# Kernel optimization log

Measured on AMD Instinct MI355X. Metric: run time of the kernel, lower is better.

## Reference

```python
import jax, jax.numpy as jnp
import numpy as np

BETA = 0.25  # commitment_beta


def setup_inputs() -> dict:
    key = jax.random.key(0)
    k1, k2 = jax.random.split(key)
    x = jax.random.normal(k1, (8, 256, 32, 32), dtype=jnp.float32)
    # nn.Embedding weight, uniform(-1/K, 1/K) in the original; use small randn-scaled init
    K, d = 4096, 256
    embed_w = jax.random.uniform(k2, (K, d), dtype=jnp.float32, minval=-1.0 / K, maxval=1.0 / K)
    return {"x": x, "embed_w": embed_w}


def reference(x, embed_w):
    B, C, H, W = x.shape
    N = H * W
    # b c h w -> b (h w) c
    xr = jnp.transpose(x, (0, 2, 3, 1)).reshape(B, N, C)
    flat = xr.reshape(B * N, C)
    dist = (-jnp.sum(flat * flat, axis=1, keepdims=True)
            - jnp.sum(embed_w * embed_w, axis=1)
            + 2.0 * jnp.einsum('nd,kd->nk', flat, embed_w))
    # temp=0.0 -> gumbel_sample degenerates to argmax
    embed_ind = jnp.argmax(dist, axis=-1).reshape(B, N)
    x_q = embed_w[embed_ind]  # [B, N, C] gather
    sg = jax.lax.stop_gradient
    loss = (BETA * jnp.mean((sg(x_q) - xr) ** 2)
            + jnp.mean((x_q - sg(xr)) ** 2))
    # straight-through estimator
    x_q = xr + sg(x_q - xr)
    # b (h w) c -> b c h w
    x_q = jnp.transpose(x_q.reshape(B, H, W, C), (0, 3, 1, 2))
    embed_ind = embed_ind.reshape(B, H, W)
    return (x_q, loss, embed_ind)
```

## Files before the change

kernel.cpp:

```cpp
#include <hip/hip_runtime.h>
#include <stdint.h>


typedef _Float16 f16;
typedef f16 half8 __attribute__((ext_vector_type(8)));
typedef float f32x4 __attribute__((ext_vector_type(4)));

__device__ __forceinline__ unsigned int sortable_f32(float v) {
    unsigned int u = __float_as_uint(v);
    return (u & 0x80000000u) ? ~u : (u | 0x80000000u);
}

__device__ __forceinline__ void gload_lds16(const void* g, void* l) {
    __builtin_amdgcn_global_load_lds(
        (const __attribute__((address_space(1))) unsigned int*)g,
        (__attribute__((address_space(3))) unsigned int*)l, 16, 0, 0);
}

__global__ void vq_pre(const float* __restrict__ x, const float* __restrict__ ew,
                       float* __restrict__ e2, float* __restrict__ negx2,
                       unsigned long long* __restrict__ cand,
                       float* __restrict__ loss_cell) {
    const int blk = blockIdx.x, tid = threadIdx.x;
    if (blk == 0 && tid == 0) *loss_cell = 0.0f;
    if (blk < 32) cand[blk * 256 + tid] = 0ull;
    if (blk < 16) {
        const int k = blk * 256 + tid;
        const float4* row = (const float4*)(ew + k * 256);
        float s = 0.0f;
#pragma unroll 8
        for (int i = 0; i < 64; ++i) {
            float4 v = row[i];
            s += v.x * v.x + v.y * v.y + v.z * v.z + v.w * v.w;
        }
        e2[k] = s;
    } else {
        const int r = (blk - 16) * 256 + tid;
        const int b = r >> 10, n = r & 1023;
        const float* px = x + b * 262144 + n;
        float s = 0.0f;
#pragma unroll 8
        for (int c = 0; c < 256; ++c) {
            float v = px[c << 10];
            s += v * v;
        }
        negx2[r] = -s;
    }
}

__global__ void split_e(const float* __restrict__ ew, f16* __restrict__ ehi, f16* __restrict__ elo) {
    const int t = blockIdx.x * 256 + threadIdx.x;
    const int k = t >> 5, g32 = t & 31;
    const float4 v0 = *(const float4*)(ew + k * 256 + g32 * 8);
    const float4 v1 = *(const float4*)(ew + k * 256 + g32 * 8 + 4);
    const float vf[8] = {v0.x, v0.y, v0.z, v0.w, v1.x, v1.y, v1.z, v1.w};
    half8 h1, h2;
#pragma unroll
    for (int j = 0; j < 8; ++j) {
        const float v = vf[j] * 4096.0f;
        const f16 a = (f16)v;
        const f16 b = (f16)(v - (float)a);
        h1[j] = a; h2[j] = b;
    }
    const int kt = k >> 7, kk = k & 127, ci = g32 >> 2, g = g32 & 3;
    const long off = ((long)((kt * 8 + ci) * 128 + kk)) * 32 + ((g ^ (kk & 3)) * 8);
    *(half8*)(ehi + off) = h1;
    *(half8*)(elo + off) = h2;
}

__global__ void split_x(const float* __restrict__ x, f16* __restrict__ xhi, f16* __restrict__ xlo) {
    __shared__ float xs[32][132];
    const int tid = threadIdx.x;
    const int ci = blockIdx.x, mt = blockIdx.y;
    const int b = mt >> 3, n0 = (mt & 7) * 128, c0 = ci * 32;
#pragma unroll
    for (int it = 0; it < 4; ++it) {
        const int idx = tid + it * 256;
        const int cc = idx >> 5, nn4 = idx & 31;
        float4 v = *(const float4*)(x + b * 262144 + (c0 + cc) * 1024 + n0 + nn4 * 4);
        *(float4*)&xs[cc][nn4 * 4] = v;
    }
    __syncthreads();
#pragma unroll
    for (int it = 0; it < 2; ++it) {
        const int idx = tid + it * 256;
        const int mm = idx & 127, g = idx >> 7;
        half8 h1, h2;
#pragma unroll
        for (int j = 0; j < 8; ++j) {
            const float v = xs[g * 8 + j][mm];
            const f16 a = (f16)v;
            const f16 bb = (f16)(v - (float)a);
            h1[j] = a; h2[j] = bb;
        }
        const long off = ((long)((mt * 8 + ci) * 128 + mm)) * 32 + ((g ^ (mm & 3)) * 8);
        *(half8*)(xhi + off) = h1;
        *(half8*)(xlo + off) = h2;
    }
}

__launch_bounds__(256, 2)
__global__ void vq_gemm(const f16* __restrict__ xhi, const f16* __restrict__ xlo,
                        const f16* __restrict__ ehi, const f16* __restrict__ elo,
                        const float* __restrict__ e2, const float* __restrict__ negx2,
                        unsigned long long* __restrict__ cand) {
    __shared__ __align__(16) f16 lds[16384];
    const int tid = threadIdx.x;
    const int kt = blockIdx.x, mt = blockIdx.y;
    const int lane = tid & 63, wave = tid >> 6;
    const int wm = wave >> 1, wk = wave & 1;
    const int col = lane & 15, quad = lane >> 4;

    f32x4 acc[4][4] = {};

    const f16* gx[2] = { xhi + (size_t)(mt * 8) * 4096, xlo + (size_t)(mt * 8) * 4096 };
    const f16* ge[2] = { ehi + (size_t)(kt * 8) * 4096, elo + (size_t)(kt * 8) * 4096 };

    int aoff[4], boff[4];
#pragma unroll
    for (int i = 0; i < 4; ++i) {
        const int m = wm * 64 + i * 16 + col;
        aoff[i] = m * 32 + ((quad ^ (m & 3)) * 8);
        const int k = wk * 64 + i * 16 + col;
        boff[i] = k * 32 + ((quad ^ (k & 3)) * 8);
    }

    for (int ci = 0; ci < 8; ++ci) {
        __syncthreads();
        const int go = ci * 4096 + tid * 8;
        char* lb = (char*)lds + (tid >> 6) * 1024;
#pragma unroll
        for (int p = 0; p < 2; ++p) {
            gload_lds16(gx[p] + go,        lb + p * 8192);
            gload_lds16(gx[p] + go + 2048, lb + p * 8192 + 4096);
            gload_lds16(ge[p] + go,        lb + 16384 + p * 8192);
            gload_lds16(ge[p] + go + 2048, lb + 16384 + p * 8192 + 4096);
        }
        __syncthreads();

        half8 ahi[4], alo[4], bhi[4], blo[4];
#pragma unroll
        for (int i = 0; i < 4; ++i) {
            ahi[i] = *(const half8*)&lds[aoff[i]];
            alo[i] = *(const half8*)&lds[4096 + aoff[i]];
            bhi[i] = *(const half8*)&lds[8192 + boff[i]];
            blo[i] = *(const half8*)&lds[12288 + boff[i]];
        }
#pragma unroll
        for (int i = 0; i < 4; ++i)
#pragma unroll
            for (int j = 0; j < 4; ++j) {
                acc[i][j] = __builtin_amdgcn_mfma_f32_16x16x32_f16(ahi[i], bhi[j], acc[i][j], 0, 0, 0);
                acc[i][j] = __builtin_amdgcn_mfma_f32_16x16x32_f16(ahi[i], blo[j], acc[i][j], 0, 0, 0);
                acc[i][j] = __builtin_amdgcn_mfma_f32_16x16x32_f16(alo[i], bhi[j], acc[i][j], 0, 0, 0);
            }
    }

    const int m0 = mt * 128 + wm * 64, k0 = kt * 128 + wk * 64;
    unsigned long long best[4][4];
#pragma unroll
    for (int i = 0; i < 4; ++i)
#pragma unroll
        for (int r = 0; r < 4; ++r) {
            const float A = negx2[m0 + i * 16 + quad * 4 + r];
            unsigned long long bk = 0ull;
#pragma unroll
            for (int j = 0; j < 4; ++j) {
                const int k = k0 + j * 16 + col;
                const float t1 = A - e2[k];
                const float dist = t1 + acc[i][j][r] * 0x1p-11f;
                const unsigned long long key =
                    ((unsigned long long)sortable_f32(dist) << 32)
                    | (unsigned long long)(unsigned int)(4095 - k);
                bk = key > bk ? key : bk;
            }
            best[i][r] = bk;
        }
#pragma unroll
    for (int i = 0; i < 4; ++i)
#pragma unroll
        for (int r = 0; r < 4; ++r) {
#pragma unroll
            for (int mask = 1; mask <= 8; mask <<= 1) {
                const unsigned long long o = __shfl_xor(best[i][r], mask, 64);
                if (o > best[i][r]) best[i][r] = o;
            }
            if (col == i * 4 + r)
                atomicMax(&cand[m0 + i * 16 + quad * 4 + r], best[i][r]);
        }
}

__global__ void vq_out(const float* __restrict__ x, const float* __restrict__ ew,
                       const unsigned long long* __restrict__ cand,
                       float* __restrict__ out) {
    __shared__ int sidx[64];
    __shared__ float wsum[4];
    const int tid = threadIdx.x;
    const int r0 = blockIdx.x * 64;
    const int b = r0 >> 10, n0 = r0 & 1023;

    if (tid < 64) {
        const int r = r0 + tid;
        const unsigned long long bk = cand[r];
        const int idx = 4095 - (int)(unsigned int)(bk & 0xFFFFFFFFull);
        sidx[tid] = idx;
        out[2097153 + r] = (float)idx;
    }
    __syncthreads();

    const int nn = tid & 63, cq = tid >> 6;
    const int myidx = sidx[nn];
    float lsum = 0.0f;
#pragma unroll 4
    for (int cb = 0; cb < 256; cb += 4) {
        const int c = cb + cq;
        const float ve = ew[myidx * 256 + c];
        const long off = (long)b * 262144 + (c << 10) + n0 + nn;
        const float vx = x[off];
        out[off] = ve;
        const float d = ve - vx;
        lsum += d * d;
    }
#pragma unroll
    for (int off = 32; off > 0; off >>= 1)
        lsum += __shfl_down(lsum, off, 64);
    const int lane = tid & 63, w = tid >> 6;
    if (lane == 0) wsum[w] = lsum;
    __syncthreads();
    if (tid == 0) {
        const float s = wsum[0] + wsum[1] + wsum[2] + wsum[3];
        atomicAdd(&out[2097152], 1.25f * (s / 2097152.0f));
    }
}

extern "C" void kernel_launch(void* const* d_in, const int* in_sizes, int n_in,
                              void* d_out, int out_size, void* d_ws, size_t ws_size,
                              hipStream_t stream) {
    const float* x  = (const float*)d_in[0];
    const float* ew = (const float*)d_in[1];
    float* out = (float*)d_out;

    float* e2 = (float*)d_ws;
    float* negx2 = e2 + 4096;
    unsigned long long* cand = (unsigned long long*)((char*)d_ws + 49152);
    f16* ehi = (f16*)((char*)d_ws + 114688);
    f16* elo = (f16*)((char*)d_ws + 114688 + 2097152);
    f16* xhi = (f16*)out;
    f16* xlo = (f16*)(out + 1048576);

    vq_pre<<<48, 256, 0, stream>>>(x, ew, e2, negx2, cand, out + 2097152);
    split_e<<<512, 256, 0, stream>>>(ew, ehi, elo);
    split_x<<<dim3(8, 64), 256, 0, stream>>>(x, xhi, xlo);
    vq_gemm<<<dim3(32, 64), 256, 0, stream>>>(xhi, xlo, ehi, elo, e2, negx2, cand);
    vq_out<<<128, 256, 0, stream>>>(x, ew, cand, out);
}
```

Before: 165.7 us.

## Merge prep kernels and fuse output gather into GEMM via last-block counter

Folds the three preprocessing kernels (norms, E split, X split) into one launch with blockIdx ranges selecting the job. When the workspace is large enough, the x hi/lo splits move into the workspace so the GEMM can finish the output itself. The last of the 32 k-tile blocks for each row tile, found with an atomic counter, gathers the codebook rows, writes the output and indices, and adds to the loss. This removes two launches and the separate vq_out pass, at the cost of fences, a serial tail on the last block per row tile, and a dependence on workspace size. The fallback path gives vq_out a wider grid.

```diff
diff --git a/kernel.cpp b/kernel.cpp
--- a/kernel.cpp
+++ b/kernel.cpp
@@ -17,15 +17,34 @@
         (__attribute__((address_space(3))) unsigned int*)l, 16, 0, 0);
 }
 
-__global__ void vq_pre(const float* __restrict__ x, const float* __restrict__ ew,
-                       float* __restrict__ e2, float* __restrict__ negx2,
-                       unsigned long long* __restrict__ cand,
-                       float* __restrict__ loss_cell) {
-    const int blk = blockIdx.x, tid = threadIdx.x;
-    if (blk == 0 && tid == 0) *loss_cell = 0.0f;
-    if (blk < 32) cand[blk * 256 + tid] = 0ull;
-    if (blk < 16) {
-        const int k = blk * 256 + tid;
+__global__ void vq_prep(const float* __restrict__ x, const float* __restrict__ ew,
+                        float* __restrict__ e2, float* __restrict__ negx2,
+                        unsigned long long* __restrict__ cand, unsigned int* __restrict__ cnt,
+                        f16* __restrict__ ehi, f16* __restrict__ elo,
+                        f16* __restrict__ xhi, f16* __restrict__ xlo,
+                        float* __restrict__ loss_cell) {
+    __shared__ float xs[32][132];
+    const int u = blockIdx.x, tid = threadIdx.x;
+    if (u < 512) {
+        const int t = u * 256 + tid;
+        const int k = t >> 5, g32 = t & 31;
+        const float4 v0 = *(const float4*)(ew + k * 256 + g32 * 8);
+        const float4 v1 = *(const float4*)(ew + k * 256 + g32 * 8 + 4);
+        const float vf[8] = {v0.x, v0.y, v0.z, v0.w, v1.x, v1.y, v1.z, v1.w};
+        half8 h1, h2;
+#pragma unroll
+        for (int j = 0; j < 8; ++j) {
+            const float v = vf[j] * 4096.0f;
+            const f16 a = (f16)v;
+            const f16 b = (f16)(v - (float)a);
+            h1[j] = a; h2[j] = b;
+        }
+        const int kt = k >> 7, kk = k & 127, ci = g32 >> 2, g = g32 & 3;
+        const long off = ((long)((kt * 8 + ci) * 128 + kk)) * 32 + ((g ^ (kk & 3)) * 8);
+        *(half8*)(ehi + off) = h1;
+        *(half8*)(elo + off) = h2;
+    } else if (u < 528) {
+        const int k = (u - 512) * 256 + tid;
         const float4* row = (const float4*)(ew + k * 256);
         float s = 0.0f;
 #pragma unroll 8
@@ -34,8 +53,13 @@
             s += v.x * v.x + v.y * v.y + v.z * v.z + v.w * v.w;
         }
         e2[k] = s;
-    } else {
-        const int r = (blk - 16) * 256 + tid;
+    } else if (u < 560) {
+        const int z = (u - 528) * 256 + tid;
+        cand[z] = 0ull;
+        if (z < 64) cnt[z] = 0u;
+        if (z == 0) *loss_cell = 0.0f;
+    } else if (u < 592) {
+        const int r = (u - 560) * 256 + tid;
         const int b = r >> 10, n = r & 1023;
         const float* px = x + b * 262144 + n;
         float s = 0.0f;
@@ -45,57 +69,34 @@
             s += v * v;
         }
         negx2[r] = -s;
-    }
-}
-
-__global__ void split_e(const float* __restrict__ ew, f16* __restrict__ ehi, f16* __restrict__ elo) {
-    const int t = blockIdx.x * 256 + threadIdx.x;
-    const int k = t >> 5, g32 = t & 31;
-    const float4 v0 = *(const float4*)(ew + k * 256 + g32 * 8);
-    const float4 v1 = *(const float4*)(ew + k * 256 + g32 * 8 + 4);
-    const float vf[8] = {v0.x, v0.y, v0.z, v0.w, v1.x, v1.y, v1.z, v1.w};
-    half8 h1, h2;
-#pragma unroll
-    for (int j = 0; j < 8; ++j) {
-        const float v = vf[j] * 4096.0f;
-        const f16 a = (f16)v;
-        const f16 b = (f16)(v - (float)a);
-        h1[j] = a; h2[j] = b;
-    }
-    const int kt = k >> 7, kk = k & 127, ci = g32 >> 2, g = g32 & 3;
-    const long off = ((long)((kt * 8 + ci) * 128 + kk)) * 32 + ((g ^ (kk & 3)) * 8);
-    *(half8*)(ehi + off) = h1;
-    *(half8*)(elo + off) = h2;
-}
-
-__global__ void split_x(const float* __restrict__ x, f16* __restrict__ xhi, f16* __restrict__ xlo) {
-    __shared__ float xs[32][132];
-    const int tid = threadIdx.x;
-    const int ci = blockIdx.x, mt = blockIdx.y;
-    const int b = mt >> 3, n0 = (mt & 7) * 128, c0 = ci * 32;
-#pragma unroll
-    for (int it = 0; it < 4; ++it) {
-        const int idx = tid + it * 256;
-        const int cc = idx >> 5, nn4 = idx & 31;
-        float4 v = *(const float4*)(x + b * 262144 + (c0 + cc) * 1024 + n0 + nn4 * 4);
-        *(float4*)&xs[cc][nn4 * 4] = v;
-    }
-    __syncthreads();
-#pragma unroll
-    for (int it = 0; it < 2; ++it) {
-        const int idx = tid + it * 256;
-        const int mm = idx & 127, g = idx >> 7;
-        half8 h1, h2;
-#pragma unroll
-        for (int j = 0; j < 8; ++j) {
-            const float v = xs[g * 8 + j][mm];
-            const f16 a = (f16)v;
-            const f16 bb = (f16)(v - (float)a);
-            h1[j] = a; h2[j] = bb;
-        }
-        const long off = ((long)((mt * 8 + ci) * 128 + mm)) * 32 + ((g ^ (mm & 3)) * 8);
-        *(half8*)(xhi + off) = h1;
-        *(half8*)(xlo + off) = h2;
+    } else {
+        const int unit = u - 592;
+        const int ci = unit & 7, mt = unit >> 3;
+        const int b = mt >> 3, n0 = (mt & 7) * 128, c0 = ci * 32;
+#pragma unroll
+        for (int it = 0; it < 4; ++it) {
+            const int idx = tid + it * 256;
+            const int cc = idx >> 5, nn4 = idx & 31;
+            float4 v = *(const float4*)(x + b * 262144 + (c0 + cc) * 1024 + n0 + nn4 * 4);
+            *(float4*)&xs[cc][nn4 * 4] = v;
+        }
+        __syncthreads();
+#pragma unroll
+        for (int it = 0; it < 2; ++it) {
+            const int idx = tid + it * 256;
+            const int mm = idx & 127, g = idx >> 7;
+            half8 h1, h2;
+#pragma unroll
+            for (int j = 0; j < 8; ++j) {
+                const float v = xs[g * 8 + j][mm];
+                const f16 a = (f16)v;
+                const f16 bb = (f16)(v - (float)a);
+                h1[j] = a; h2[j] = bb;
+            }
+            const long off = ((long)((mt * 8 + ci) * 128 + mm)) * 32 + ((g ^ (mm & 3)) * 8);
+            *(half8*)(xhi + off) = h1;
+            *(half8*)(xlo + off) = h2;
+        }
     }
 }
 
@@ -103,7 +104,9 @@
 __global__ void vq_gemm(const f16* __restrict__ xhi, const f16* __restrict__ xlo,
                         const f16* __restrict__ ehi, const f16* __restrict__ elo,
                         const float* __restrict__ e2, const float* __restrict__ negx2,
-                        unsigned long long* __restrict__ cand) {
+                        unsigned long long* __restrict__ cand, unsigned int* __restrict__ cnt,
+                        const float* __restrict__ x, const float* __restrict__ ew,
+                        float* __restrict__ out, int do_tail) {
     __shared__ __align__(16) f16 lds[16384];
     const int tid = threadIdx.x;
     const int kt = blockIdx.x, mt = blockIdx.y;
@@ -128,7 +131,7 @@
     for (int ci = 0; ci < 8; ++ci) {
         __syncthreads();
         const int go = ci * 4096 + tid * 8;
-        char* lb = (char*)lds + (tid >> 6) * 1024;
+        char* lb = (char*)lds + wave * 1024;
 #pragma unroll
         for (int p = 0; p < 2; ++p) {
             gload_lds16(gx[p] + go,        lb + p * 8192);
@@ -138,26 +141,25 @@
         }
         __syncthreads();
 
-        half8 ahi[4], alo[4], bhi[4], blo[4];
+        half8 ahi4[4], alo4[4], bhi4[4], blo4[4];
 #pragma unroll
         for (int i = 0; i < 4; ++i) {
-            ahi[i] = *(const half8*)&lds[aoff[i]];
-            alo[i] = *(const half8*)&lds[4096 + aoff[i]];
-            bhi[i] = *(const half8*)&lds[8192 + boff[i]];
-            blo[i] = *(const half8*)&lds[12288 + boff[i]];
+            ahi4[i] = *(const half8*)&lds[aoff[i]];
+            alo4[i] = *(const half8*)&lds[4096 + aoff[i]];
+            bhi4[i] = *(const half8*)&lds[8192 + boff[i]];
+            blo4[i] = *(const half8*)&lds[12288 + boff[i]];
         }
 #pragma unroll
         for (int i = 0; i < 4; ++i)
 #pragma unroll
             for (int j = 0; j < 4; ++j) {
-                acc[i][j] = __builtin_amdgcn_mfma_f32_16x16x32_f16(ahi[i], bhi[j], acc[i][j], 0, 0, 0);
-                acc[i][j] = __builtin_amdgcn_mfma_f32_16x16x32_f16(ahi[i], blo[j], acc[i][j], 0, 0, 0);
-                acc[i][j] = __builtin_amdgcn_mfma_f32_16x16x32_f16(alo[i], bhi[j], acc[i][j], 0, 0, 0);
+                acc[i][j] = __builtin_amdgcn_mfma_f32_16x16x32_f16(ahi4[i], bhi4[j], acc[i][j], 0, 0, 0);
+                acc[i][j] = __builtin_amdgcn_mfma_f32_16x16x32_f16(ahi4[i], blo4[j], acc[i][j], 0, 0, 0);
+                acc[i][j] = __builtin_amdgcn_mfma_f32_16x16x32_f16(alo4[i], bhi4[j], acc[i][j], 0, 0, 0);
             }
     }
 
     const int m0 = mt * 128 + wm * 64, k0 = kt * 128 + wk * 64;
-    unsigned long long best[4][4];
 #pragma unroll
     for (int i = 0; i < 4; ++i)
 #pragma unroll
@@ -172,22 +174,60 @@
                 const unsigned long long key =
                     ((unsigned long long)sortable_f32(dist) << 32)
                     | (unsigned long long)(unsigned int)(4095 - k);
-                bk = key > bk ? key : bk;
+                if (key > bk) bk = key;
             }
-            best[i][r] = bk;
-        }
-#pragma unroll
-    for (int i = 0; i < 4; ++i)
-#pragma unroll
-        for (int r = 0; r < 4; ++r) {
 #pragma unroll
             for (int mask = 1; mask <= 8; mask <<= 1) {
-                const unsigned long long o = __shfl_xor(best[i][r], mask, 64);
-                if (o > best[i][r]) best[i][r] = o;
+                const unsigned long long o = __shfl_xor(bk, mask, 64);
+                if (o > bk) bk = o;
             }
             if (col == i * 4 + r)
-                atomicMax(&cand[m0 + i * 16 + quad * 4 + r], best[i][r]);
-        }
+                atomicMax(&cand[m0 + i * 16 + quad * 4 + r], bk);
+        }
+
+    if (!do_tail) return;
+
+    __threadfence();
+    __syncthreads();
+    __shared__ unsigned int sOld;
+    if (tid == 0) sOld = atomicAdd(&cnt[mt], 1u);
+    __syncthreads();
+    if (sOld != 31u) return;
+    __threadfence();
+
+    const int r0 = mt * 128;
+    const int b = r0 >> 10, n0 = r0 & 1023;
+    int* sidx = (int*)lds;
+    float* wsum = (float*)((char*)lds + 1024);
+    if (tid < 128) {
+        const int r = r0 + tid;
+        const unsigned long long bk =
+            __hip_atomic_load(&cand[r], __ATOMIC_RELAXED, __HIP_MEMORY_SCOPE_AGENT);
+        const int idx = 4095 - (int)(unsigned int)(bk & 0xFFFFFFFFull);
+        sidx[tid] = idx;
+        out[2097153 + r] = (float)idx;
+    }
+    __syncthreads();
+    const int nn = tid & 127, ch = tid >> 7;
+    const int myidx = sidx[nn];
+    float lsum = 0.0f;
+#pragma unroll 4
+    for (int cb = 0; cb < 128; ++cb) {
+        const int c = ch * 128 + cb;
+        const float ve = ew[myidx * 256 + c];
+        const long off = (long)b * 262144 + (c << 10) + n0 + nn;
+        const float vx = x[off];
+        out[off] = ve;
+        const float d = ve - vx;
+        lsum += d * d;
+    }
+#pragma unroll
+    for (int o = 32; o > 0; o >>= 1) lsum += __shfl_down(lsum, o, 64);
+    if ((tid & 63) == 0) wsum[tid >> 6] = lsum;
+    __syncthreads();
+    if (tid == 0)
+        atomicAdd(&out[2097152],
+                  1.25f * ((wsum[0] + wsum[1] + wsum[2] + wsum[3]) / 2097152.0f));
 }
 
 __global__ void vq_out(const float* __restrict__ x, const float* __restrict__ ew,
@@ -197,23 +237,22 @@
     __shared__ float wsum[4];
     const int tid = threadIdx.x;
     const int r0 = blockIdx.x * 64;
+    const int cq0 = blockIdx.y * 64;
     const int b = r0 >> 10, n0 = r0 & 1023;
-
     if (tid < 64) {
         const int r = r0 + tid;
         const unsigned long long bk = cand[r];
         const int idx = 4095 - (int)(unsigned int)(bk & 0xFFFFFFFFull);
         sidx[tid] = idx;
-        out[2097153 + r] = (float)idx;
-    }
-    __syncthreads();
-
+        if (cq0 == 0) out[2097153 + r] = (float)idx;
+    }
+    __syncthreads();
     const int nn = tid & 63, cq = tid >> 6;
     const int myidx = sidx[nn];
     float lsum = 0.0f;
 #pragma unroll 4
-    for (int cb = 0; cb < 256; cb += 4) {
-        const int c = cb + cq;
+    for (int cb = 0; cb < 16; ++cb) {
+        const int c = cq0 + cb * 4 + cq;
         const float ve = ew[myidx * 256 + c];
         const long off = (long)b * 262144 + (c << 10) + n0 + nn;
         const float vx = x[off];
@@ -222,15 +261,12 @@
         lsum += d * d;
     }
 #pragma unroll
-    for (int off = 32; off > 0; off >>= 1)
-        lsum += __shfl_down(lsum, off, 64);
-    const int lane = tid & 63, w = tid >> 6;
-    if (lane == 0) wsum[w] = lsum;
-    __syncthreads();
-    if (tid == 0) {
-        const float s = wsum[0] + wsum[1] + wsum[2] + wsum[3];
-        atomicAdd(&out[2097152], 1.25f * (s / 2097152.0f));
-    }
+    for (int o = 32; o > 0; o >>= 1) lsum += __shfl_down(lsum, o, 64);
+    if ((tid & 63) == 0) wsum[tid >> 6] = lsum;
+    __syncthreads();
+    if (tid == 0)
+        atomicAdd(&out[2097152],
+                  1.25f * ((wsum[0] + wsum[1] + wsum[2] + wsum[3]) / 2097152.0f));
 }
 
 extern "C" void kernel_launch(void* const* d_in, const int* in_sizes, int n_in,
@@ -243,14 +279,25 @@
     float* e2 = (float*)d_ws;
     float* negx2 = e2 + 4096;
     unsigned long long* cand = (unsigned long long*)((char*)d_ws + 49152);
-    f16* ehi = (f16*)((char*)d_ws + 114688);
-    f16* elo = (f16*)((char*)d_ws + 114688 + 2097152);
-    f16* xhi = (f16*)out;
-    f16* xlo = (f16*)(out + 1048576);
-
-    vq_pre<<<48, 256, 0, stream>>>(x, ew, e2, negx2, cand, out + 2097152);
-    split_e<<<512, 256, 0, stream>>>(ew, ehi, elo);
-    split_x<<<dim3(8, 64), 256, 0, stream>>>(x, xhi, xlo);
-    vq_gemm<<<dim3(32, 64), 256, 0, stream>>>(xhi, xlo, ehi, elo, e2, negx2, cand);
-    vq_out<<<128, 256, 0, stream>>>(x, ew, cand, out);
-}
+    unsigned int* cnt = (unsigned int*)((char*)d_ws + 114688);
+    f16* ehi = (f16*)((char*)d_ws + 114944);
+    f16* elo = (f16*)((char*)d_ws + 114944 + 2097152);
+
+    const size_t need = 114944ull + 4ull * 2097152ull + 2ull * 4194304ull;
+    if (ws_size >= need) {
+        f16* xhi = (f16*)((char*)d_ws + 114944 + 2 * 2097152);
+        f16* xlo = (f16*)((char*)d_ws + 114944 + 2 * 2097152 + 4194304);
+        vq_prep<<<1104, 256, 0, stream>>>(x, ew, e2, negx2, cand, cnt,
+                                          ehi, elo, xhi, xlo, out + 2097152);
+        vq_gemm<<<dim3(32, 64), 256, 0, stream>>>(xhi, xlo, ehi, elo, e2, negx2,
+                                                  cand, cnt, x, ew, out, 1);
+    } else {
+        f16* xhi = (f16*)out;
+        f16* xlo = (f16*)(out + 1048576);
+        vq_prep<<<1104, 256, 0, stream>>>(x, ew, e2, negx2, cand, cnt,
+                                          ehi, elo, xhi, xlo, out + 2097152);
+        vq_gemm<<<dim3(32, 64), 256, 0, stream>>>(xhi, xlo, ehi, elo, e2, negx2,
+                                                  cand, cnt, x, ew, out, 0);
+        vq_out<<<dim3(128, 4), 256, 0, stream>>>(x, ew, cand, out);
+    }
+}
```

New measurement: 421.8 us. +154.5%, slower.
